# Optimization experiments

Measured on AMD Instinct MI355X. Metric: run time of the kernel, lower is better.

Reference implementation:

```python
import jax, jax.numpy as jnp
import numpy as np

# FoldLayer config (matches init_kwargs)
K = 3            # kernel_size
S = 2            # strides
D = 1            # dilation_rate
OUT_H, OUT_W = 128, 128   # target output size
PAD = K // 2     # 'same' padding -> 1
B, GH, GW, C = 16, 64, 64, 128   # batch, patch-grid h/w, channels
H, W = OUT_H + 2 * PAD, OUT_W + 2 * PAD  # padded fold canvas


def setup_inputs() -> dict:
    key = jax.random.key(0)
    # compressed patches layout: last dim is [k*k, C] kernel-major,
    # as implied by reshape(patches, [-1, h*w, k*k, C]) in call()
    patches = jax.random.normal(key, (B, GH, GW, K * K * C), dtype=jnp.float32)
    return {"patches": patches}


def reference(patches) -> jnp.ndarray:
    # (B, GH, GW, K*K*C) -> (B, GH, GW, K, K, C), kernel-major per call()'s reshape
    p = patches.reshape(B, GH, GW, K, K, C)
    out = jnp.zeros((B, H, W, C), dtype=patches.dtype)
    # Overlap-add scatter: out[b, y*S + i*D, x*S + j*D, c] += p[b, y, x, i, j, c]
    # K*K = 9 fixed small iterations; each is a strided-slice add (vectorized over B,GH,GW,C).
    for i in range(K):
        for j in range(K):
            oi, oj = i * D, j * D
            out = out.at[:, oi:oi + GH * S:S, oj:oj + GW * S:S, :].add(p[:, :, :, i, j, :])
    # Crop the 'same' padding, equivalent to tf.slice in call()
    return out[:, PAD:PAD + OUT_H, PAD:PAD + OUT_W, :]
```

## Files before the change

kernel.cpp:

```cpp
#include <hip/hip_runtime.h>


#define GH 64
#define GW 64

typedef float v4f __attribute__((ext_vector_type(4)));

__global__ __launch_bounds__(256) void fold_gather_kernel(
    const v4f* __restrict__ p, v4f* __restrict__ out) {
    const int PSTRIDE = 288;
    const int BSTRIDE_IN  = GH * GW * PSTRIDE;
    const int BSTRIDE_OUT = 128 * 128 * 32;

    int tid = blockIdx.x * 256 + threadIdx.x;
    int c4  = tid & 31;
    int pix = tid >> 5;
    int ow  = pix & 127;
    int oh  = (pix >> 7) & 127;
    int b   = pix >> 14;

    int hp = oh + 1, wp = ow + 1;
    int yA = hp >> 1, iA = hp & 1;
    int xA = wp >> 1, jA = wp & 1;
    bool hA = (yA < GH);
    bool hB = (iA == 0);
    bool wA = (xA < GW);
    bool wB = (jA == 0);

    int rowA = (b * GH + yA) * GW;
    int rowB = rowA - GW;

    v4f acc0 = {0.f, 0.f, 0.f, 0.f};
    v4f acc1 = {0.f, 0.f, 0.f, 0.f};
    auto add = [&](bool valid, int row, int xx, int ii, int jj) {
        if (valid) {
            int idx = (row + xx) * PSTRIDE + (ii * 3 + jj) * 32 + c4;
            v4f v0 = __builtin_nontemporal_load(&p[idx]);
            v4f v1 = __builtin_nontemporal_load(&p[idx + 8 * BSTRIDE_IN]);
            acc0 += v0;
            acc1 += v1;
        }
    };
    add(hA && wA, rowA, xA,     iA, jA);
    add(hA && wB, rowA, xA - 1, iA, 2);
    add(hB && wA, rowB, xA,     2,  jA);
    add(hB && wB, rowB, xA - 1, 2,  2);

    int oidx = pix * 32 + c4;
    __builtin_nontemporal_store(acc0, &out[oidx]);
    __builtin_nontemporal_store(acc1, &out[oidx + 8 * BSTRIDE_OUT]);
}

extern "C" void kernel_launch(void* const* d_in, const int* in_sizes, int n_in,
                              void* d_out, int out_size, void* d_ws, size_t ws_size,
                              hipStream_t stream) {
    const v4f* p = (const v4f*)d_in[0];
    v4f* out = (v4f*)d_out;
    int total_threads = out_size / 8;
    dim3 block(256);
    dim3 grid(total_threads / 256);
    fold_gather_kernel<<<grid, block, 0, stream>>>(p, out);
}
```

Measured before the change: 414.9 us.

## Compute a 2x2 output block per patch cell in fold kernel

```diff
diff --git a/kernel.cpp b/kernel.cpp
--- a/kernel.cpp
+++ b/kernel.cpp
@@ -6,49 +6,66 @@
 
 typedef float v4f __attribute__((ext_vector_type(4)));
 
-__global__ __launch_bounds__(256) void fold_gather_kernel(
+__global__ __launch_bounds__(256) void fold_block_kernel(
     const v4f* __restrict__ p, v4f* __restrict__ out) {
-    const int PSTRIDE = 288;
+    const int PSTRIDE     = 288;
+    const int ROWSTRIDE   = GW * PSTRIDE;
     const int BSTRIDE_IN  = GH * GW * PSTRIDE;
     const int BSTRIDE_OUT = 128 * 128 * 32;
 
     int tid = blockIdx.x * 256 + threadIdx.x;
-    int c4  = tid & 31;
-    int pix = tid >> 5;
-    int ow  = pix & 127;
-    int oh  = (pix >> 7) & 127;
-    int b   = pix >> 14;
+    int c4 = tid & 31;
+    int bx = (tid >> 5) & 63;
+    int by = (tid >> 11) & 63;
+    int b  = tid >> 17;
 
-    int hp = oh + 1, wp = ow + 1;
-    int yA = hp >> 1, iA = hp & 1;
-    int xA = wp >> 1, jA = wp & 1;
-    bool hA = (yA < GH);
-    bool hB = (iA == 0);
-    bool wA = (xA < GW);
-    bool wB = (jA == 0);
+    bool tOk = (by < GH - 1);
+    bool uOk = (bx < GW - 1);
 
-    int rowA = (b * GH + yA) * GW;
-    int rowB = rowA - GW;
+    const v4f* q0 = p + ((b * GH + by) * GW + bx) * PSTRIDE + c4;
+    const v4f* q1 = q0 + 8 * BSTRIDE_IN;
 
-    v4f acc0 = {0.f, 0.f, 0.f, 0.f};
-    v4f acc1 = {0.f, 0.f, 0.f, 0.f};
-    auto add = [&](bool valid, int row, int xx, int ii, int jj) {
-        if (valid) {
-            int idx = (row + xx) * PSTRIDE + (ii * 3 + jj) * 32 + c4;
-            v4f v0 = __builtin_nontemporal_load(&p[idx]);
-            v4f v1 = __builtin_nontemporal_load(&p[idx + 8 * BSTRIDE_IN]);
-            acc0 += v0;
-            acc1 += v1;
+    v4f a00 = __builtin_nontemporal_load(q0 + 4 * 32);
+    v4f c00 = __builtin_nontemporal_load(q1 + 4 * 32);
+    v4f a01 = __builtin_nontemporal_load(q0 + 5 * 32);
+    v4f c01 = __builtin_nontemporal_load(q1 + 5 * 32);
+    v4f a10 = __builtin_nontemporal_load(q0 + 7 * 32);
+    v4f c10 = __builtin_nontemporal_load(q1 + 7 * 32);
+    v4f a11 = __builtin_nontemporal_load(q0 + 8 * 32);
+    v4f c11 = __builtin_nontemporal_load(q1 + 8 * 32);
+
+    if (uOk) {
+        const v4f* r0 = q0 + PSTRIDE;
+        const v4f* r1 = q1 + PSTRIDE;
+        a01 += __builtin_nontemporal_load(r0 + 3 * 32);
+        c01 += __builtin_nontemporal_load(r1 + 3 * 32);
+        a11 += __builtin_nontemporal_load(r0 + 6 * 32);
+        c11 += __builtin_nontemporal_load(r1 + 6 * 32);
+    }
+    if (tOk) {
+        const v4f* r0 = q0 + ROWSTRIDE;
+        const v4f* r1 = q1 + ROWSTRIDE;
+        a10 += __builtin_nontemporal_load(r0 + 1 * 32);
+        c10 += __builtin_nontemporal_load(r1 + 1 * 32);
+        a11 += __builtin_nontemporal_load(r0 + 2 * 32);
+        c11 += __builtin_nontemporal_load(r1 + 2 * 32);
+        if (uOk) {
+            a11 += __builtin_nontemporal_load(r0 + ROWSTRIDE - ROWSTRIDE + PSTRIDE + 0 * 32);
+            c11 += __builtin_nontemporal_load(r1 + PSTRIDE + 0 * 32);
         }
-    };
-    add(hA && wA, rowA, xA,     iA, jA);
-    add(hA && wB, rowA, xA - 1, iA, 2);
-    add(hB && wA, rowB, xA,     2,  jA);
-    add(hB && wB, rowB, xA - 1, 2,  2);
+    }
 
-    int oidx = pix * 32 + c4;
-    __builtin_nontemporal_store(acc0, &out[oidx]);
-    __builtin_nontemporal_store(acc1, &out[oidx + 8 * BSTRIDE_OUT]);
+    int o = ((b * 128 + 2 * by) * 128 + 2 * bx) * 32 + c4;
+    v4f* w0 = out + o;
+    v4f* w1 = w0 + 8 * BSTRIDE_OUT;
+    __builtin_nontemporal_store(a00, w0);
+    __builtin_nontemporal_store(a01, w0 + 32);
+    __builtin_nontemporal_store(a10, w0 + 128 * 32);
+    __builtin_nontemporal_store(a11, w0 + 128 * 32 + 32);
+    __builtin_nontemporal_store(c00, w1);
+    __builtin_nontemporal_store(c01, w1 + 32);
+    __builtin_nontemporal_store(c10, w1 + 128 * 32);
+    __builtin_nontemporal_store(c11, w1 + 128 * 32 + 32);
 }
 
 extern "C" void kernel_launch(void* const* d_in, const int* in_sizes, int n_in,
@@ -56,8 +73,7 @@
                               hipStream_t stream) {
     const v4f* p = (const v4f*)d_in[0];
     v4f* out = (v4f*)d_out;
-    int total_threads = out_size / 8;
     dim3 block(256);
-    dim3 grid(total_threads / 256);
-    fold_gather_kernel<<<grid, block, 0, stream>>>(p, out);
+    dim3 grid(1048576 / 256);
+    fold_block_kernel<<<grid, block, 0, stream>>>(p, out);
 }
```

Result: no change. 408.8 us (-1.5%).
